# Optimization experiments

Hardware: AMD Instinct MI355X
Metric: run time of the kernel (lower is better)

The kernel has to match this reference:

```python
import jax, jax.numpy as jnp
import numpy as np

B, N = 32, 50000
E = 200000
D, D_LG = 64, 256
M_ALL, M_MEM = 100000, 80000
NUM_VI_SEG = 80000


def _dense(key, din, dout):
    k1, k2 = jax.random.split(key)
    lim = 1.0 / np.sqrt(din)
    W = jax.random.uniform(k1, (din, dout), jnp.float32, -lim, lim)
    b = jax.random.uniform(k2, (dout,), jnp.float32, -lim, lim)
    return W, b


def setup_inputs() -> dict:
    key = jax.random.key(0)
    ks = jax.random.split(key, 16)
    rng = np.random.RandomState(0)

    eg = np.sort(rng.randint(0, B, E)).astype(np.int32)
    vi = rng.randint(0, N, E).astype(np.int32)
    vj = rng.randint(0, N, E).astype(np.int32)
    rel = rng.randint(0, 200, E).astype(np.int32)
    seg_vi = np.sort(rng.randint(0, NUM_VI_SEG, E)).astype(np.int32)
    seg_vj = rng.randint(0, E, E).astype(np.int32)
    e2vi = rng.randint(0, M_ALL, E).astype(np.int32)
    e2vj = rng.randint(0, M_ALL, E).astype(np.int32)
    scanned_edges = jnp.asarray(np.stack([eg, vi, vj, rel, seg_vi, seg_vj, e2vi, e2vj], axis=1))

    new_idx = np.sort(rng.choice(M_ALL, M_MEM, replace=False)).astype(np.int32)[:, None]

    W_h, b_h = _dense(ks[0], D, D)
    W_hlg, b_hlg = _dense(ks[1], D_LG, D)
    W_rlg, b_rlg = _dense(ks[2], D_LG, D)
    Wl0, bl0 = _dense(ks[3], D, D)
    Wr0, br0 = _dense(ks[4], D, D)
    Wl1, bl1 = _dense(ks[5], 2 * D, D)
    Wr1, br1 = _dense(ks[6], 2 * D, D)

    return {
        'node_attention': jax.random.uniform(ks[7], (B, N), jnp.float32),
        'edges_y': jax.random.uniform(ks[8], (E,), jnp.float32),
        'hidden_uncon': jax.random.normal(ks[9], (1, N, D_LG), jnp.float32),
        'hidden_con': jax.random.normal(ks[10], (M_MEM, D), jnp.float32),
        'query_head_emb': jax.random.normal(ks[11], (B, D_LG), jnp.float32),
        'query_rel_emb': jax.random.normal(ks[12], (B, D_LG), jnp.float32),
        'W_h': W_h, 'b_h': b_h, 'W_hlg': W_hlg, 'b_hlg': b_hlg,
        'W_rlg': W_rlg, 'b_rlg': b_rlg,
        'Wl0': Wl0, 'bl0': bl0, 'Wr0': Wr0, 'br0': br0,
        'Wl1': Wl1, 'bl1': bl1, 'Wr1': Wr1, 'br1': br1,
        'scanned_edges': scanned_edges,
        'new_idx_for_memorized': jnp.asarray(new_idx),
        'n_memorized_and_scanned_nodes': M_ALL,
    }


def _segment_softmax(logits, seg, num_seg):
    # numerically-stable sparse softmax over sorted vi-segments
    m = jax.ops.segment_max(logits, seg, num_segments=num_seg)
    e = jnp.exp(logits - m[seg])
    s = jax.ops.segment_sum(e, seg, num_segments=num_seg)
    return e / s[seg]


def reference(node_attention, edges_y, hidden_uncon, hidden_con,
              query_head_emb, query_rel_emb,
              W_h, b_h, W_hlg, b_hlg, W_rlg, b_rlg,
              Wl0, bl0, Wr0, br0, Wl1, bl1, Wr1, br1,
              scanned_edges, new_idx_for_memorized, n_memorized_and_scanned_nodes):
    Bv, Nv = node_attention.shape
    eg = scanned_edges[:, 0]
    vi = scanned_edges[:, 1]
    vj = scanned_edges[:, 2]
    seg_vi = scanned_edges[:, 4]
    e2vi = scanned_edges[:, 6]
    e2vj = scanned_edges[:, 7]

    # proj_for_hidden, scatter memorized states to memorized+scanned slots
    hc = jnp.tanh(hidden_con @ W_h + b_h)                        # M_mem x D
    hc_full = jnp.zeros((n_memorized_and_scanned_nodes, hc.shape[-1]), hc.dtype)
    hc_full = hc_full.at[new_idx_for_memorized[:, 0]].set(hc)    # M_all x D

    hu = jnp.tanh(hidden_uncon @ W_hlg + b_hlg)
    qh = jnp.tanh(query_head_emb @ W_hlg + b_hlg)                # B x D (use_ent_emb)
    qr = jnp.tanh(query_rel_emb @ W_rlg + b_rlg)                 # B x D
    qv = qh + qr

    # node2edge gathers (context = conditioned + unconditioned hidden)
    h_vi = hc_full[e2vi] + hu[0, vi]                             # E x D
    h_vj = hc_full[e2vj] + hu[0, vj]                             # E x D
    q_e = qv[eg]                                                 # E x D

    # transition_fn G with interact [[[0],[1]], [[0,2],[1,2]]]
    l0 = jnp.tanh(h_vi @ Wl0 + bl0)
    r0 = jnp.tanh(h_vj @ Wr0 + br0)
    l1 = jnp.tanh(jnp.concatenate([h_vi, q_e], -1) @ Wl1 + bl1)
    r1 = jnp.tanh(jnp.concatenate([h_vj, q_e], -1) @ Wr1 + br1)
    logits = jnp.sum(l0 * r0, -1) + jnp.sum(l1 * r1, -1)         # E

    # neighbor softmax at vi, modulated by edges_y
    trans = _segment_softmax(logits, seg_vi, NUM_VI_SEG) * edges_y

    # flow: gather attention at vi, aggregate(sum) scatter to (eg_idx, vj)
    flow = node_attention[eg, vi] * trans
    new_att = jnp.zeros((Bv, Nv), flow.dtype).at[eg, vj].add(flow)
    return new_att
```

## Files before the change

kernel.cpp:

```cpp
#include <hip/hip_runtime.h>


typedef __attribute__((ext_vector_type(8))) short s16x8;
typedef __attribute__((ext_vector_type(4))) float f32x4;
typedef __attribute__((ext_vector_type(8))) unsigned short u16x8;

__device__ __forceinline__ float fast_tanh(float x) {
    float e = __expf(2.0f * x);
    return 1.0f - 2.0f * __builtin_amdgcn_rcpf(e + 1.0f);
}

__device__ __forceinline__ unsigned short bf16r(float f) {
    unsigned int u = __float_as_uint(f);
    u = (u + 0x7fffu + ((u >> 16) & 1u)) >> 16;
    return (unsigned short)u;
}
__device__ __forceinline__ float bf16f(unsigned short h) {
    return __uint_as_float(((unsigned int)h) << 16);
}
__device__ __forceinline__ float blo(unsigned int u) {
    return __uint_as_float(u << 16);
}
__device__ __forceinline__ float bhi(unsigned int u) {
    return __uint_as_float(u & 0xffff0000u);
}

__device__ __forceinline__ int saddr(int row, int chunk) {
    return (row << 6) + ((chunk ^ (row & 7)) << 2);
}

__global__ void k_scatter_inv(const int* __restrict__ new_idx, int* __restrict__ inv, int M) {
    int i = blockIdx.x * blockDim.x + threadIdx.x;
    if (i < M) inv[new_idx[i]] = i;
}

__global__ void k_pack(const float* __restrict__ Wl0, const float* __restrict__ Wl1,
                       const float* __restrict__ Wr0, const float* __restrict__ Wr1,
                       unsigned short* __restrict__ Bp) {
    int tid = blockIdx.x * blockDim.x + threadIdx.x;
    if (tid >= 2048) return;
    int lane = tid & 63;
    int ks = (tid >> 6) & 1;
    int g = tid >> 7;
    int col = g * 16 + (lane & 15);
    int kb = ks * 32 + (lane >> 4) * 8;
    const float* W = (col < 64) ? Wl0 : (col < 128) ? Wl1 : (col < 192) ? Wr0 : Wr1;
    int c = col & 63;
    unsigned short hi[8], lo[8];
    #pragma unroll
    for (int i = 0; i < 8; ++i) {
        float w = W[(kb + i) * 64 + c];
        hi[i] = bf16r(w);
        lo[i] = bf16r(w - bf16f(hi[i]));
    }
    unsigned short* dh = Bp + (size_t)tid * 8;
    unsigned short* dl = Bp + 16384 + (size_t)tid * 8;
    #pragma unroll
    for (int i = 0; i < 8; ++i) { dh[i] = hi[i]; dl[i] = lo[i]; }
}

__global__ void k_q(const float* __restrict__ qhe, const float* __restrict__ qre,
                    const float* __restrict__ W_hlg, const float* __restrict__ b_hlg,
                    const float* __restrict__ W_rlg, const float* __restrict__ b_rlg,
                    const float* __restrict__ Wl1, const float* __restrict__ bl1,
                    const float* __restrict__ Wr1, const float* __restrict__ br1,
                    float* __restrict__ ql1b, float* __restrict__ qr1b) {
    __shared__ float qv_s[64];
    int b = blockIdx.x, d = threadIdx.x;
    float ah = 0.f, ar = 0.f;
    for (int k = 0; k < 256; ++k) {
        ah += qhe[b * 256 + k] * W_hlg[k * 64 + d];
        ar += qre[b * 256 + k] * W_rlg[k * 64 + d];
    }
    qv_s[d] = fast_tanh(ah + b_hlg[d]) + fast_tanh(ar + b_rlg[d]);
    __syncthreads();
    float a1 = 0.f, a2 = 0.f;
    for (int k = 0; k < 64; ++k) {
        float v = qv_s[k];
        a1 += v * Wl1[(64 + k) * 64 + d];
        a2 += v * Wr1[(64 + k) * 64 + d];
    }
    ql1b[b * 64 + d] = a1 + bl1[d];
    qr1b[b * 64 + d] = a2 + br1[d];
}

__global__ __launch_bounds__(256, 6) void k_tab(
        const float* __restrict__ Xc, const float* __restrict__ Xu,
        const float* __restrict__ W_h, const float* __restrict__ b_h,
        const float* __restrict__ W_hlg, const float* __restrict__ b_hlg,
        const float* __restrict__ bl0, const float* __restrict__ br0,
        const unsigned short* __restrict__ Bp,
        unsigned short* __restrict__ Ahc, unsigned short* __restrict__ Ahu,
        int M, int N, int HCB) {
    __shared__ float s[64 * 64];
    __shared__ unsigned short dstage[16 * 264];
    unsigned short* hhi = reinterpret_cast<unsigned short*>(s);

    const int t = threadIdx.x;
    const int wu = __builtin_amdgcn_readfirstlane(t >> 6);
    const int lane = t & 63;
    const bool hc = ((int)blockIdx.x < HCB);

    float acc1[16];
    #pragma unroll
    for (int c = 0; c < 16; ++c) acc1[c] = 0.f;

    int base, rows;
    const float* bias;
    unsigned short* table;

    if (hc) {
        base = blockIdx.x * 64;
        rows = (M - base < 64) ? (M - base) : 64;
        bias = b_h;
        table = Ahc;
        #pragma unroll
        for (int i = 0; i < 4; ++i) {
            int f = i * 256 + t;
            int r = f >> 4, ch = f & 15;
            float4 v = make_float4(0.f, 0.f, 0.f, 0.f);
            if (r < rows) v = *reinterpret_cast<const float4*>(Xc + (size_t)(base + r) * 64 + (ch << 2));
            *reinterpret_cast<float4*>(&s[saddr(r, ch)]) = v;
        }
        __syncthreads();
        for (int k4 = 0; k4 < 16; ++k4) {
            float4 xv = *reinterpret_cast<const float4*>(&s[saddr(lane, k4)]);
            #pragma unroll
            for (int kk = 0; kk < 4; ++kk) {
                float xk = (&xv.x)[kk];
                const float* wrow = W_h + (k4 * 4 + kk) * 64 + wu * 16;
                #pragma unroll
                for (int c = 0; c < 16; ++c) acc1[c] = __builtin_fmaf(xk, wrow[c], acc1[c]);
            }
        }
    } else {
        base = ((int)blockIdx.x - HCB) * 64;
        rows = (N - base < 64) ? (N - base) : 64;
        bias = b_hlg;
        table = Ahu;
        for (int kc = 0; kc < 4; ++kc) {
            __syncthreads();
            #pragma unroll
            for (int i = 0; i < 4; ++i) {
                int f = i * 256 + t;
                int r = f >> 4, ch = f & 15;
                float4 v = make_float4(0.f, 0.f, 0.f, 0.f);
                if (r < rows)
                    v = *reinterpret_cast<const float4*>(Xu + (size_t)(base + r) * 256 + kc * 64 + (ch << 2));
                *reinterpret_cast<float4*>(&s[saddr(r, ch)]) = v;
            }
            __syncthreads();
            const float* Wb = W_hlg + (size_t)kc * 64 * 64;
            for (int k4 = 0; k4 < 16; ++k4) {
                float4 xv = *reinterpret_cast<const float4*>(&s[saddr(lane, k4)]);
                #pragma unroll
                for (int kk = 0; kk < 4; ++kk) {
                    float xk = (&xv.x)[kk];
                    const float* wrow = Wb + (k4 * 4 + kk) * 64 + wu * 16;
                    #pragma unroll
                    for (int c = 0; c < 16; ++c) acc1[c] = __builtin_fmaf(xk, wrow[c], acc1[c]);
                }
            }
        }
    }

    __syncthreads();
    {
        unsigned short hi[16];
        #pragma unroll
        for (int c = 0; c < 16; ++c)
            hi[c] = bf16r(fast_tanh(acc1[c] + bias[wu * 16 + c]));
        int o = lane * 68 + wu * 16;
        #pragma unroll
        for (int c = 0; c < 16; ++c) hhi[o + c] = hi[c];
    }
    __syncthreads();

    const s16x8* Bph = reinterpret_cast<const s16x8*>(Bp);
    const s16x8* Bpl = reinterpret_cast<const s16x8*>(Bp + 16384);
    const int l15 = lane & 15, l4 = lane >> 4;
    for (int rt = 0; rt < 4; ++rt) {
        int arow = (rt * 16 + l15) * 68 + l4 * 8;
        s16x8 a0v = *reinterpret_cast<const s16x8*>(&hhi[arow]);
        s16x8 a1v = *reinterpret_cast<const s16x8*>(&hhi[arow + 32]);
        #pragma unroll
        for (int ct = 0; ct < 4; ++ct) {
            int g = wu * 4 + ct;
            s16x8 bh0 = Bph[(g * 2 + 0) * 64 + lane];
            s16x8 bh1 = Bph[(g * 2 + 1) * 64 + lane];
            s16x8 bl0v = Bpl[(g * 2 + 0) * 64 + lane];
            s16x8 bl1v = Bpl[(g * 2 + 1) * 64 + lane];
            f32x4 acc = {0.f, 0.f, 0.f, 0.f};
            acc = __builtin_amdgcn_mfma_f32_16x16x32_bf16(a0v, bh0, acc, 0, 0, 0);
            acc = __builtin_amdgcn_mfma_f32_16x16x32_bf16(a1v, bh1, acc, 0, 0, 0);
            acc = __builtin_amdgcn_mfma_f32_16x16x32_bf16(a0v, bl0v, acc, 0, 0, 0);
            acc = __builtin_amdgcn_mfma_f32_16x16x32_bf16(a1v, bl1v, acc, 0, 0, 0);
            float badd = 0.f;
            if (!hc) {
                if (g < 4) badd = bl0[g * 16 + l15];
                else if (g >= 8 && g < 12) badd = br0[(g - 8) * 16 + l15];
            }
            int side = g >> 3, which = (g >> 2) & 1;
            int x = (g & 3) * 16 + l15;
            int pos = side * 128 + x * 2 + which;
            #pragma unroll
            for (int r = 0; r < 4; ++r)
                dstage[(l4 * 4 + r) * 264 + pos] = bf16r(acc[r] + badd);
        }
        __syncthreads();
        #pragma unroll
        for (int it = 0; it < 2; ++it) {
            int f = (it * 256 + t) * 8;
            int row = f >> 8, off = f & 255;
            u16x8 v = *reinterpret_cast<const u16x8*>(&dstage[row * 264 + off]);
            int grow = rt * 16 + row;
            if (grow < rows)
                *reinterpret_cast<u16x8*>(&table[(size_t)(base + grow) * 256 + off]) = v;
        }
        __syncthreads();
    }
}

__global__ void k_edge(const int* __restrict__ se, const int* __restrict__ inv,
                       const unsigned int* __restrict__ Ahc, const unsigned int* __restrict__ Ahu,
                       const float* __restrict__ ql1b, const float* __restrict__ qr1b,
                       float* __restrict__ trans, float* __restrict__ psum,
                       int E, int ZROW) {
    int tid = blockIdx.x * blockDim.x + threadIdx.x;
    int e = tid >> 4;
    int sl = tid & 15;
    if (e >= E) return;
    const int4* sr = reinterpret_cast<const int4*>(se + (size_t)e * 8);
    int4 ra = sr[0], rb = sr[1];
    int eg = ra.x, vi = ra.y, vj = ra.z, seg = rb.x, e2vi = rb.z, e2vj = rb.w;
    int ii = inv[e2vi]; ii = (ii < 0) ? ZROW : ii;
    int ij = inv[e2vj]; ij = (ij < 0) ? ZROW : ij;
    uint4 a  = *reinterpret_cast<const uint4*>(Ahc + (size_t)ii * 128 + sl * 4);
    uint4 b  = *reinterpret_cast<const uint4*>(Ahu + (size_t)vi * 128 + sl * 4);
    uint4 c  = *reinterpret_cast<const uint4*>(Ahc + (size_t)ij * 128 + 64 + sl * 4);
    uint4 d4 = *reinterpret_cast<const uint4*>(Ahu + (size_t)vj * 128 + 64 + sl * 4);
    float4 q1 = *reinterpret_cast<const float4*>(ql1b + eg * 64 + sl * 4);
    float4 q2 = *reinterpret_cast<const float4*>(qr1b + eg * 64 + sl * 4);
    float acc = 0.f;
    #pragma unroll
    for (int j = 0; j < 4; ++j) {
        unsigned int av = (&a.x)[j], bv = (&b.x)[j];
        unsigned int cv = (&c.x)[j], dv = (&d4.x)[j];
        float l0 = fast_tanh(blo(av) + blo(bv));
        float l1 = fast_tanh(bhi(av) + bhi(bv) + (&q1.x)[j]);
        float r0 = fast_tanh(blo(cv) + blo(dv));
        float r1 = fast_tanh(bhi(cv) + bhi(dv) + (&q2.x)[j]);
        acc = __builtin_fmaf(l0, r0, acc);
        acc = __builtin_fmaf(l1, r1, acc);
    }
    #pragma unroll
    for (int off = 8; off; off >>= 1) acc += __shfl_xor(acc, off);
    if (sl == 0) {
        float ex = __expf(acc);
        trans[e] = ex;
        atomicAdd(&psum[seg], ex);
    }
}

__global__ void k_final(const int* __restrict__ se, const float* __restrict__ trans,
                        const float* __restrict__ psum, const float* __restrict__ ey,
                        const float* __restrict__ natt, float* __restrict__ out,
                        int E, int N) {
    int e = blockIdx.x * blockDim.x + threadIdx.x;
    if (e >= E) return;
    const int* row = se + (size_t)e * 8;
    int eg = row[0], vi = row[1], vj = row[2], seg = row[4];
    float t = trans[e] * __builtin_amdgcn_rcpf(psum[seg]) * ey[e] * natt[(size_t)eg * N + vi];
    atomicAdd(&out[(size_t)eg * N + vj], t);
}

extern "C" void kernel_launch(void* const* d_in, const int* in_sizes, int n_in,
                              void* d_out, int out_size, void* d_ws, size_t ws_size,
                              hipStream_t stream) {
    const float* natt  = (const float*)d_in[0];
    const float* ey    = (const float*)d_in[1];
    const float* h_unc = (const float*)d_in[2];
    const float* h_con = (const float*)d_in[3];
    const float* qhe   = (const float*)d_in[4];
    const float* qre   = (const float*)d_in[5];
    const float* W_h   = (const float*)d_in[6];
    const float* b_h   = (const float*)d_in[7];
    const float* W_hlg = (const float*)d_in[8];
    const float* b_hlg = (const float*)d_in[9];
    const float* W_rlg = (const float*)d_in[10];
    const float* b_rlg = (const float*)d_in[11];
    const float* Wl0   = (const float*)d_in[12];
    const float* bl0   = (const float*)d_in[13];
    const float* Wr0   = (const float*)d_in[14];
    const float* br0   = (const float*)d_in[15];
    const float* Wl1   = (const float*)d_in[16];
    const float* bl1   = (const float*)d_in[17];
    const float* Wr1   = (const float*)d_in[18];
    const float* br1   = (const float*)d_in[19];
    const int* se      = (const int*)d_in[20];
    const int* new_idx = (const int*)d_in[21];

    const int B     = 32;
    const int N     = in_sizes[0] / B;
    const int E     = in_sizes[20] / 8;
    const int M_MEM = in_sizes[21];
    const int M_ALL = 100000;
    const int NSEG  = 80000;

    char* ws = (char*)d_ws;
    size_t off = 0;
    unsigned short* Ahc = (unsigned short*)(ws + off);  off += (size_t)(M_MEM + 1) * 256 * 2;
    unsigned short* Ahu = (unsigned short*)(ws + off);  off += (size_t)N * 256 * 2;
    int* inv = (int*)(ws + off);            off += (size_t)M_ALL * 4;
    float* trans = (float*)(ws + off);      off += (size_t)E * 4;
    float* psum = (float*)(ws + off);       off += (size_t)NSEG * 4;
    float* ql1b = (float*)(ws + off);       off += (size_t)B * 64 * 4;
    float* qr1b = (float*)(ws + off);       off += (size_t)B * 64 * 4;
    unsigned short* Bpack = (unsigned short*)(ws + off); off += (size_t)2 * 16384 * 2;

    hipMemsetAsync(d_out, 0, (size_t)out_size * 4, stream);
    hipMemsetAsync(inv, 0xFF, (size_t)M_ALL * 4, stream);
    hipMemsetAsync(psum, 0, (size_t)NSEG * 4, stream);
    hipMemsetAsync(Ahc + (size_t)M_MEM * 256, 0, 256 * 2, stream);

    const int HCB = (M_MEM + 63) / 64;
    const int HUB = (N + 63) / 64;

    k_scatter_inv<<<(M_MEM + 255) / 256, 256, 0, stream>>>(new_idx, inv, M_MEM);
    k_pack<<<8, 256, 0, stream>>>(Wl0, Wl1, Wr0, Wr1, Bpack);
    k_q<<<B, 64, 0, stream>>>(qhe, qre, W_hlg, b_hlg, W_rlg, b_rlg,
                              Wl1, bl1, Wr1, br1, ql1b, qr1b);
    k_tab<<<HCB + HUB, 256, 0, stream>>>(h_con, h_unc, W_h, b_h, W_hlg, b_hlg,
                                         bl0, br0, Bpack, Ahc, Ahu, M_MEM, N, HCB);
    k_edge<<<((size_t)E * 16 + 255) / 256, 256, 0, stream>>>(se, inv, (const unsigned int*)Ahc,
                                                (const unsigned int*)Ahu, ql1b, qr1b,
                                                trans, psum, E, M_MEM);
    k_final<<<(E + 255) / 256, 256, 0, stream>>>(se, trans, psum, ey, natt, (float*)d_out, E, N);
}
```

Before: 141.6 us.

## Move first-layer table GEMM from scalar FMA to split-bf16 MFMA

Replaces the scalar fp32 FMA loop that computes tanh(X@W_h+b) and tanh(Xu@W_hlg+b) in k_tab with bf16 MFMA instructions. Both operands are split into hi/lo bf16 parts and three products are accumulated to keep close to fp32 accuracy. New pack kernels pre-layout W_h and W_hlg into MFMA fragment order, and the LDS staging now holds bf16 hi/lo planes. Launch bounds rise to 8 waves per SIMD. The aim is to cut ALU time in the table build, at the cost of extra pack launches and some precision loss from dropping the lo*lo term.

```diff
diff --git a/kernel.cpp b/kernel.cpp
--- a/kernel.cpp
+++ b/kernel.cpp
@@ -4,6 +4,7 @@
 typedef __attribute__((ext_vector_type(8))) short s16x8;
 typedef __attribute__((ext_vector_type(4))) float f32x4;
 typedef __attribute__((ext_vector_type(8))) unsigned short u16x8;
+typedef __attribute__((ext_vector_type(4))) unsigned short u16x4;
 
 __device__ __forceinline__ float fast_tanh(float x) {
     float e = __expf(2.0f * x);
@@ -23,10 +24,6 @@
 }
 __device__ __forceinline__ float bhi(unsigned int u) {
     return __uint_as_float(u & 0xffff0000u);
-}
-
-__device__ __forceinline__ int saddr(int row, int chunk) {
-    return (row << 6) + ((chunk ^ (row & 7)) << 2);
 }
 
 __global__ void k_scatter_inv(const int* __restrict__ new_idx, int* __restrict__ inv, int M) {
@@ -46,17 +43,32 @@
     int kb = ks * 32 + (lane >> 4) * 8;
     const float* W = (col < 64) ? Wl0 : (col < 128) ? Wl1 : (col < 192) ? Wr0 : Wr1;
     int c = col & 63;
-    unsigned short hi[8], lo[8];
     #pragma unroll
     for (int i = 0; i < 8; ++i) {
         float w = W[(kb + i) * 64 + c];
-        hi[i] = bf16r(w);
-        lo[i] = bf16r(w - bf16f(hi[i]));
-    }
-    unsigned short* dh = Bp + (size_t)tid * 8;
-    unsigned short* dl = Bp + 16384 + (size_t)tid * 8;
-    #pragma unroll
-    for (int i = 0; i < 8; ++i) { dh[i] = hi[i]; dl[i] = lo[i]; }
+        unsigned short hi = bf16r(w);
+        unsigned short lo = bf16r(w - bf16f(hi));
+        Bp[(size_t)tid * 8 + i] = hi;
+        Bp[16384 + (size_t)tid * 8 + i] = lo;
+    }
+}
+
+__global__ void k_pack1(const float* __restrict__ W, unsigned short* __restrict__ dh,
+                        unsigned short* __restrict__ dl, int nflat) {
+    int tid = blockIdx.x * blockDim.x + threadIdx.x;
+    if (tid >= nflat) return;
+    int lane = tid & 63;
+    int f = tid >> 6;
+    int kb = (f >> 2) * 32 + ((lane >> 4) * 8);
+    int col = (f & 3) * 16 + (lane & 15);
+    #pragma unroll
+    for (int i = 0; i < 8; ++i) {
+        float w = W[(kb + i) * 64 + col];
+        unsigned short hi = bf16r(w);
+        unsigned short lo = bf16r(w - bf16f(hi));
+        dh[(size_t)tid * 8 + i] = hi;
+        dl[(size_t)tid * 8 + i] = lo;
+    }
 }
 
 __global__ void k_q(const float* __restrict__ qhe, const float* __restrict__ qre,
@@ -84,105 +96,100 @@
     qr1b[b * 64 + d] = a2 + br1[d];
 }
 
-__global__ __launch_bounds__(256, 6) void k_tab(
+__global__ __launch_bounds__(256, 8) void k_tab(
         const float* __restrict__ Xc, const float* __restrict__ Xu,
-        const float* __restrict__ W_h, const float* __restrict__ b_h,
-        const float* __restrict__ W_hlg, const float* __restrict__ b_hlg,
+        const float* __restrict__ b_h, const float* __restrict__ b_hlg,
         const float* __restrict__ bl0, const float* __restrict__ br0,
         const unsigned short* __restrict__ Bp,
+        const unsigned short* __restrict__ WhH, const unsigned short* __restrict__ WhL,
+        const unsigned short* __restrict__ WgH, const unsigned short* __restrict__ WgL,
         unsigned short* __restrict__ Ahc, unsigned short* __restrict__ Ahu,
         int M, int N, int HCB) {
-    __shared__ float s[64 * 64];
-    __shared__ unsigned short dstage[16 * 264];
-    unsigned short* hhi = reinterpret_cast<unsigned short*>(s);
+    __shared__ unsigned short lds_a[64 * 72];
+    __shared__ unsigned short lds_b[64 * 72];
 
     const int t = threadIdx.x;
     const int wu = __builtin_amdgcn_readfirstlane(t >> 6);
     const int lane = t & 63;
+    const int l15 = lane & 15, l4 = lane >> 4;
     const bool hc = ((int)blockIdx.x < HCB);
 
-    float acc1[16];
-    #pragma unroll
-    for (int c = 0; c < 16; ++c) acc1[c] = 0.f;
-
-    int base, rows;
-    const float* bias;
-    unsigned short* table;
-
-    if (hc) {
-        base = blockIdx.x * 64;
-        rows = (M - base < 64) ? (M - base) : 64;
-        bias = b_h;
-        table = Ahc;
+    const int base = hc ? (int)blockIdx.x * 64 : ((int)blockIdx.x - HCB) * 64;
+    const int lim  = hc ? M : N;
+    const int rows = (lim - base < 64) ? (lim - base) : 64;
+    const int nkc  = hc ? 1 : 4;
+    const int ldx  = hc ? 64 : 256;
+    const float* __restrict__ X    = hc ? Xc : Xu;
+    const float* __restrict__ bias = hc ? b_h : b_hlg;
+    unsigned short* __restrict__ table = hc ? Ahc : Ahu;
+    const s16x8* __restrict__ WH = reinterpret_cast<const s16x8*>(hc ? WhH : WgH);
+    const s16x8* __restrict__ WL = reinterpret_cast<const s16x8*>(hc ? WhL : WgL);
+
+    f32x4 acc1m[4];
+    #pragma unroll
+    for (int rt = 0; rt < 4; ++rt) acc1m[rt] = (f32x4){0.f, 0.f, 0.f, 0.f};
+
+    for (int kc = 0; kc < nkc; ++kc) {
+        __syncthreads();
         #pragma unroll
         for (int i = 0; i < 4; ++i) {
             int f = i * 256 + t;
             int r = f >> 4, ch = f & 15;
             float4 v = make_float4(0.f, 0.f, 0.f, 0.f);
-            if (r < rows) v = *reinterpret_cast<const float4*>(Xc + (size_t)(base + r) * 64 + (ch << 2));
-            *reinterpret_cast<float4*>(&s[saddr(r, ch)]) = v;
+            if (r < rows)
+                v = *reinterpret_cast<const float4*>(X + (size_t)(base + r) * ldx + kc * 64 + ch * 4);
+            u16x4 vh, vl;
+            #pragma unroll
+            for (int j = 0; j < 4; ++j) {
+                float x = (&v.x)[j];
+                unsigned short h16 = (unsigned short)(__float_as_uint(x) >> 16);
+                vh[j] = h16;
+                vl[j] = bf16r(x - bf16f(h16));
+            }
+            *reinterpret_cast<u16x4*>(&lds_a[r * 72 + ch * 4]) = vh;
+            *reinterpret_cast<u16x4*>(&lds_b[r * 72 + ch * 4]) = vl;
         }
         __syncthreads();
-        for (int k4 = 0; k4 < 16; ++k4) {
-            float4 xv = *reinterpret_cast<const float4*>(&s[saddr(lane, k4)]);
+        int fb = (kc * 2) * 4 + wu;
+        s16x8 bh0 = WH[fb * 64 + lane],       bl0v = WL[fb * 64 + lane];
+        s16x8 bh1 = WH[(fb + 4) * 64 + lane], bl1v = WL[(fb + 4) * 64 + lane];
+        #pragma unroll
+        for (int rt = 0; rt < 4; ++rt) {
+            int rowa = (rt * 16 + l15) * 72 + l4 * 8;
+            s16x8 ah0 = *reinterpret_cast<const s16x8*>(&lds_a[rowa]);
+            s16x8 al0 = *reinterpret_cast<const s16x8*>(&lds_b[rowa]);
+            s16x8 ah1 = *reinterpret_cast<const s16x8*>(&lds_a[rowa + 32]);
+            s16x8 al1 = *reinterpret_cast<const s16x8*>(&lds_b[rowa + 32]);
+            acc1m[rt] = __builtin_amdgcn_mfma_f32_16x16x32_bf16(ah0, bh0,  acc1m[rt], 0, 0, 0);
+            acc1m[rt] = __builtin_amdgcn_mfma_f32_16x16x32_bf16(ah0, bl0v, acc1m[rt], 0, 0, 0);
+            acc1m[rt] = __builtin_amdgcn_mfma_f32_16x16x32_bf16(al0, bh0,  acc1m[rt], 0, 0, 0);
+            acc1m[rt] = __builtin_amdgcn_mfma_f32_16x16x32_bf16(ah1, bh1,  acc1m[rt], 0, 0, 0);
+            acc1m[rt] = __builtin_amdgcn_mfma_f32_16x16x32_bf16(ah1, bl1v, acc1m[rt], 0, 0, 0);
+            acc1m[rt] = __builtin_amdgcn_mfma_f32_16x16x32_bf16(al1, bh1,  acc1m[rt], 0, 0, 0);
+        }
+    }
+    __syncthreads();
+
+    {
+        float bv = bias[wu * 16 + l15];
+        #pragma unroll
+        for (int rt = 0; rt < 4; ++rt) {
             #pragma unroll
-            for (int kk = 0; kk < 4; ++kk) {
-                float xk = (&xv.x)[kk];
-                const float* wrow = W_h + (k4 * 4 + kk) * 64 + wu * 16;
-                #pragma unroll
-                for (int c = 0; c < 16; ++c) acc1[c] = __builtin_fmaf(xk, wrow[c], acc1[c]);
+            for (int r = 0; r < 4; ++r) {
+                int row = rt * 16 + l4 * 4 + r;
+                lds_a[row * 68 + wu * 16 + l15] = bf16r(fast_tanh(acc1m[rt][r] + bv));
             }
         }
-    } else {
-        base = ((int)blockIdx.x - HCB) * 64;
-        rows = (N - base < 64) ? (N - base) : 64;
-        bias = b_hlg;
-        table = Ahu;
-        for (int kc = 0; kc < 4; ++kc) {
-            __syncthreads();
-            #pragma unroll
-            for (int i = 0; i < 4; ++i) {
-                int f = i * 256 + t;
-                int r = f >> 4, ch = f & 15;
-                float4 v = make_float4(0.f, 0.f, 0.f, 0.f);
-                if (r < rows)
-                    v = *reinterpret_cast<const float4*>(Xu + (size_t)(base + r) * 256 + kc * 64 + (ch << 2));
-                *reinterpret_cast<float4*>(&s[saddr(r, ch)]) = v;
-            }
-            __syncthreads();
-            const float* Wb = W_hlg + (size_t)kc * 64 * 64;
-            for (int k4 = 0; k4 < 16; ++k4) {
-                float4 xv = *reinterpret_cast<const float4*>(&s[saddr(lane, k4)]);
-                #pragma unroll
-                for (int kk = 0; kk < 4; ++kk) {
-                    float xk = (&xv.x)[kk];
-                    const float* wrow = Wb + (k4 * 4 + kk) * 64 + wu * 16;
-                    #pragma unroll
-                    for (int c = 0; c < 16; ++c) acc1[c] = __builtin_fmaf(xk, wrow[c], acc1[c]);
-                }
-            }
-        }
-    }
-
-    __syncthreads();
-    {
-        unsigned short hi[16];
-        #pragma unroll
-        for (int c = 0; c < 16; ++c)
-            hi[c] = bf16r(fast_tanh(acc1[c] + bias[wu * 16 + c]));
-        int o = lane * 68 + wu * 16;
-        #pragma unroll
-        for (int c = 0; c < 16; ++c) hhi[o + c] = hi[c];
     }
     __syncthreads();
 
     const s16x8* Bph = reinterpret_cast<const s16x8*>(Bp);
     const s16x8* Bpl = reinterpret_cast<const s16x8*>(Bp + 16384);
-    const int l15 = lane & 15, l4 = lane >> 4;
+    unsigned short* dstage = lds_b;
     for (int rt = 0; rt < 4; ++rt) {
         int arow = (rt * 16 + l15) * 68 + l4 * 8;
-        s16x8 a0v = *reinterpret_cast<const s16x8*>(&hhi[arow]);
-        s16x8 a1v = *reinterpret_cast<const s16x8*>(&hhi[arow + 32]);
+        s16x8 a0v = *reinterpret_cast<const s16x8*>(&lds_a[arow]);
+        s16x8 a1v = *reinterpret_cast<const s16x8*>(&lds_a[arow + 32]);
         #pragma unroll
         for (int ct = 0; ct < 4; ++ct) {
             int g = wu * 4 + ct;
@@ -317,6 +324,10 @@
     float* ql1b = (float*)(ws + off);       off += (size_t)B * 64 * 4;
     float* qr1b = (float*)(ws + off);       off += (size_t)B * 64 * 4;
     unsigned short* Bpack = (unsigned short*)(ws + off); off += (size_t)2 * 16384 * 2;
+    unsigned short* WhH = (unsigned short*)(ws + off);   off += (size_t)4096 * 2;
+    unsigned short* WhL = (unsigned short*)(ws + off);   off += (size_t)4096 * 2;
+    unsigned short* WgH = (unsigned short*)(ws + off);   off += (size_t)16384 * 2;
+    unsigned short* WgL = (unsigned short*)(ws + off);   off += (size_t)16384 * 2;
 
     hipMemsetAsync(d_out, 0, (size_t)out_size * 4, stream);
     hipMemsetAsync(inv, 0xFF, (size_t)M_ALL * 4, stream);
@@ -328,10 +339,13 @@
 
     k_scatter_inv<<<(M_MEM + 255) / 256, 256, 0, stream>>>(new_idx, inv, M_MEM);
     k_pack<<<8, 256, 0, stream>>>(Wl0, Wl1, Wr0, Wr1, Bpack);
+    k_pack1<<<2, 256, 0, stream>>>(W_h, WhH, WhL, 512);
+    k_pack1<<<8, 256, 0, stream>>>(W_hlg, WgH, WgL, 2048);
     k_q<<<B, 64, 0, stream>>>(qhe, qre, W_hlg, b_hlg, W_rlg, b_rlg,
                               Wl1, bl1, Wr1, br1, ql1b, qr1b);
-    k_tab<<<HCB + HUB, 256, 0, stream>>>(h_con, h_unc, W_h, b_h, W_hlg, b_hlg,
-                                         bl0, br0, Bpack, Ahc, Ahu, M_MEM, N, HCB);
+    k_tab<<<HCB + HUB, 256, 0, stream>>>(h_con, h_unc, b_h, b_hlg, bl0, br0,
+                                         Bpack, WhH, WhL, WgH, WgL,
+                                         Ahc, Ahu, M_MEM, N, HCB);
     k_edge<<<((size_t)E * 16 + 255) / 256, 256, 0, stream>>>(se, inv, (const unsigned int*)Ahc,
                                                 (const unsigned int*)Ahu, ql1b, qr1b,
                                                 trans, psum, E, M_MEM);
```

After: 159.3 us. 12.5% more time.
